# Kernel optimization log

Hardware: AMD Instinct MI355X
Metric: run time of the kernel (lower is better)

The kernel has to match this reference:

```python
import jax, jax.numpy as jnp
import numpy as np

B, P, T, K = 8, 64, 63, 2        # scenes, proposals/scene, text tokens, target proposals/scene
D, DFF, L = 512, 2048, 2         # d_model, ffn dim, encoder layers
V, NC = 30522, 18                # vocab, classes
DPT, DWD = 1536, 768             # point feats, word feats
S = P + T


def _ln(x, g, b):
    m = x.mean(-1, keepdims=True)
    v = ((x - m) ** 2).mean(-1, keepdims=True)
    return (x - m) * jax.lax.rsqrt(v + 1e-5) * g + b


def _encode(x, mask, enc):
    # post-norm TransformerEncoderLayer (torch default), dropout=0 (eval)
    (qkv_w, qkv_b, out_w, out_b, ln1_g, ln1_b,
     ff1_w, ff1_b, ff2_w, ff2_b, ln2_g, ln2_b) = enc
    for l in range(L):
        qkv = x @ qkv_w[l] + qkv_b[l]
        q, k, v = jnp.split(qkv, 3, axis=-1)
        s = q @ k.T * (1.0 / np.sqrt(D)) + mask
        a = jax.nn.softmax(s, axis=-1) @ v
        x = _ln(x + a @ out_w[l] + out_b[l], ln1_g[l], ln1_b[l])
        f = jax.nn.relu(x @ ff1_w[l] + ff1_b[l]) @ ff2_w[l] + ff2_b[l]
        x = _ln(x + f, ln2_g[l], ln2_b[l])
    return x


def _seq2seq_mask():
    # boxes attend to boxes only; text attends to all boxes + causal text
    i = jnp.arange(S)[:, None]
    j = jnp.arange(S)[None, :]
    allowed = (j < P) | ((i >= P) & (j <= i))
    return jnp.where(allowed, 0.0, -1e9).astype(jnp.float32)


def setup_inputs():
    ks = iter(jax.random.split(jax.random.key(0), 48))

    def nrm(shape, s=0.02):
        return jax.random.normal(next(ks), shape, jnp.float32) * s

    return dict(
        instances=jax.random.normal(next(ks), (B * P, DPT), jnp.float32),
        text_embeddings=jax.random.normal(next(ks), (B, T, DWD), jnp.float32),
        target_proposals=jax.random.randint(next(ks), (B, K), 0, P),
        target_word_ids=jax.random.randint(next(ks), (B, T + 1), 0, V),
        target_classes=jax.random.randint(next(ks), (B,), 0, NC),
        Wi1=nrm((DPT, 1024)), bi1=jnp.zeros((1024,)),
        Wi2=nrm((1024, D)), bi2=jnp.zeros((D,)),
        Ww=nrm((DWD, D)), bw=jnp.zeros((D,)),
        qkv_w=nrm((L, D, 3 * D)), qkv_b=jnp.zeros((L, 3 * D)),
        out_w=nrm((L, D, D)), out_b=jnp.zeros((L, D)),
        ln1_g=jnp.ones((L, D)), ln1_b=jnp.zeros((L, D)),
        ff1_w=nrm((L, D, DFF)), ff1_b=jnp.zeros((L, DFF)),
        ff2_w=nrm((L, DFF, D)), ff2_b=jnp.zeros((L, D)),
        ln2_g=jnp.ones((L, D)), ln2_b=jnp.zeros((L, D)),
        grd_w1=nrm((D, 256)), grd_b1=jnp.zeros((256,)),
        grd_w2=nrm((256, 1)), grd_b2=jnp.zeros((1,)),
        cls_w1=nrm((D, 256)), cls_b1=jnp.zeros((256,)),
        cls_w2=nrm((256, NC)), cls_b2=jnp.zeros((NC,)),
        cap_w1=nrm((D, DWD)), cap_b1=jnp.zeros((DWD,)),
        cap_w2=nrm((DWD, V)), cap_b2=jnp.zeros((V,)),
    )


def reference(instances, text_embeddings, target_proposals, target_word_ids,
              target_classes, Wi1, bi1, Wi2, bi2, Ww, bw, qkv_w, qkv_b, out_w,
              out_b, ln1_g, ln1_b, ff1_w, ff1_b, ff2_w, ff2_b, ln2_g, ln2_b,
              grd_w1, grd_b1, grd_w2, grd_b2, cls_w1, cls_b1, cls_w2, cls_b2,
              cap_w1, cap_b1, cap_w2, cap_b2):
    enc = (qkv_w, qkv_b, out_w, out_b, ln1_g, ln1_b,
           ff1_w, ff1_b, ff2_w, ff2_b, ln2_g, ln2_b)
    box = ((instances @ Wi1 + bi1) @ Wi2 + bi2).reshape(B, P, D)
    txt = text_embeddings @ Ww + bw                                   # [B,T,D]
    # ---- VG branch (unmasked encoder) ----
    vg = jnp.concatenate([box, txt + box.mean(1, keepdims=True)], axis=1)
    out_vg = jax.vmap(lambda x: _encode(x, 0.0, enc))(vg)             # [B,S,D]
    match_scores = (((out_vg[:, :P] @ grd_w1 + grd_b1) @ grd_w2 + grd_b2)
                    .squeeze(-1))                                     # [B,P]
    cls_scores = (out_vg[:, P] @ cls_w1 + cls_b1) @ cls_w2 + cls_b2   # [B,NC]
    # ---- DC branch (seq2seq mask), vmapped over scenes x target proposals ----
    tgt_box = jnp.take_along_axis(box, target_proposals[:, :, None], axis=1)
    cue = txt[:, None] + tgt_box[:, :, None]                          # [B,K,T,D]
    dc = jnp.concatenate(
        [jnp.broadcast_to(box[:, None], (B, K, P, D)), cue], axis=2)  # [B,K,S,D]
    mask = _seq2seq_mask()
    out_dc = jax.vmap(jax.vmap(lambda x: _encode(x, mask, enc)))(dc)
    dc_scores = (out_dc[:, :, P:] @ cap_w1 + cap_b1) @ cap_w2 + cap_b2  # [B,K,T,V]
    # ---- losses ----
    tgt = jnp.zeros((B, P)).at[jnp.arange(B)[:, None], target_proposals].set(1.0 / K)
    match_loss = (-(tgt * jax.nn.log_softmax(match_scores, -1)).sum(-1)).mean()
    cls_lp = jax.nn.log_softmax(cls_scores, -1)
    cls_loss = -jnp.take_along_axis(cls_lp, target_classes[:, None], 1).mean()
    wid = jnp.broadcast_to(target_word_ids[:, None, 1:T + 1], (B, K, T))
    dc_lp = jnp.take_along_axis(jax.nn.log_softmax(dc_scores, -1),
                                wid[..., None], axis=3)[..., 0]       # [B,K,T]
    dc_loss = (-dc_lp.mean(-1)).sum(-1).mean()   # sum over proposals, mean over scenes
    return (match_scores, match_loss, cls_scores, cls_loss, dc_scores, dc_loss)
```

## Files before the change

kernel.cpp:

```cpp
#include <hip/hip_runtime.h>
#include <hip/hip_bf16.h>


typedef __hip_bfloat16 bf16;
typedef __attribute__((ext_vector_type(8))) __bf16 bf16x8;
typedef __attribute__((ext_vector_type(4))) float floatx4;

#define NB 8
#define NP 64
#define NT 63
#define NK 2
#define ND 512
#define NDFF 2048
#define NV 30522
#define NNC 18
#define NS 127
#define NSEQ 24
#define NROWS (NSEQ*NS)

#define OUT_MS 0
#define OUT_MLOSS 512
#define OUT_CS 513
#define OUT_CLOSS 657
#define OUT_DC 658
#define OUT_DCLOSS 30766834

#define C2M 1008
#define C2N 30522
#define C2K 768
#define C2NT 239
#define C2H  478

__device__ __forceinline__ float bflo(unsigned u){ return __uint_as_float(u << 16); }
__device__ __forceinline__ float bfhi(unsigned u){ return __uint_as_float(u & 0xffff0000u); }

__device__ __forceinline__ void gload16(const void* g, void* l) {
    __builtin_amdgcn_global_load_lds(
        (const __attribute__((address_space(1))) unsigned*)g,
        (__attribute__((address_space(3))) unsigned*)l, 16, 0, 0);
}

#define LDSS 40

__global__ __launch_bounds__(256) void gemm_kernel(
    const bf16* __restrict__ A, const bf16* __restrict__ WT,
    const float* __restrict__ bias, const bf16* __restrict__ resid,
    bf16* __restrict__ C, int M, int N, int K, int relu)
{
    __shared__ bf16 As[64 * LDSS];
    __shared__ bf16 Bs[64 * LDSS];
    const int tid = threadIdx.x;
    const int m0 = blockIdx.x * 64;
    const int n0 = blockIdx.y * 64;
    const int lane = tid & 63;
    const int wave = tid >> 6;
    const int wm = (wave >> 1) * 32, wn = (wave & 1) * 32;
    const int quad = lane >> 4, r = lane & 15;
    const int lrow = tid >> 2;
    const int lk = (tid & 3) * 8;
    const int arow = m0 + lrow;
    const int brow = n0 + lrow;

    floatx4 acc[2][2] = {};

    for (int k0 = 0; k0 < K; k0 += 32) {
        __syncthreads();
        int4 av = {0,0,0,0}, bv = {0,0,0,0};
        if (arow < M) av = *(const int4*)(A  + (size_t)arow * K + k0 + lk);
        if (brow < N) bv = *(const int4*)(WT + (size_t)brow * K + k0 + lk);
        *(int4*)(&As[lrow * LDSS + lk]) = av;
        *(int4*)(&Bs[lrow * LDSS + lk]) = bv;
        __syncthreads();

        bf16x8 a0 = *(const bf16x8*)(&As[(wm + r)      * LDSS + quad * 8]);
        bf16x8 a1 = *(const bf16x8*)(&As[(wm + 16 + r) * LDSS + quad * 8]);
        bf16x8 b0 = *(const bf16x8*)(&Bs[(wn + r)      * LDSS + quad * 8]);
        bf16x8 b1 = *(const bf16x8*)(&Bs[(wn + 16 + r) * LDSS + quad * 8]);
        acc[0][0] = __builtin_amdgcn_mfma_f32_16x16x32_bf16(a0, b0, acc[0][0], 0, 0, 0);
        acc[0][1] = __builtin_amdgcn_mfma_f32_16x16x32_bf16(a0, b1, acc[0][1], 0, 0, 0);
        acc[1][0] = __builtin_amdgcn_mfma_f32_16x16x32_bf16(a1, b0, acc[1][0], 0, 0, 0);
        acc[1][1] = __builtin_amdgcn_mfma_f32_16x16x32_bf16(a1, b1, acc[1][1], 0, 0, 0);
    }

    #pragma unroll
    for (int ti = 0; ti < 2; ++ti)
    #pragma unroll
    for (int tj = 0; tj < 2; ++tj) {
        int col = n0 + wn + tj * 16 + r;
        if (col >= N) continue;
        float bvv = bias ? bias[col] : 0.f;
        #pragma unroll
        for (int rr = 0; rr < 4; ++rr) {
            int row = m0 + wm + ti * 16 + quad * 4 + rr;
            if (row >= M) continue;
            float v = acc[ti][tj][rr] + bvv;
            if (resid) v += (float)resid[(size_t)row * N + col];
            if (relu)  v = v > 0.f ? v : 0.f;
            C[(size_t)row * N + col] = __float2bfloat16(v);
        }
    }
}

__global__ __launch_bounds__(256) void gemm128_kernel(
    const bf16* __restrict__ A, const bf16* __restrict__ WT,
    const float* __restrict__ bias, const bf16* __restrict__ resid,
    bf16* __restrict__ C, int M, int N, int K, int relu)
{
    __shared__ bf16 As[128 * 32];
    __shared__ bf16 Bs[128 * 32];
    const int tid = threadIdx.x;
    const int m0 = blockIdx.x * 128;
    const int n0 = blockIdx.y * 128;
    const int lane = tid & 63, wave = tid >> 6;
    const int quad = lane >> 4, r = lane & 15;
    const int wm = (wave >> 1) * 64, wn = (wave & 1) * 64;
    const int srow0 = wave * 32 + (lane >> 2);
    const int srow1 = srow0 + 16;
    const int sk = (lane & 3) * 8;
    const int ar0 = min(m0 + srow0, M - 1), ar1 = min(m0 + srow1, M - 1);
    const int br0 = min(n0 + srow0, N - 1), br1 = min(n0 + srow1, N - 1);
    bf16* lA = As + srow0 * 32 + sk;
    bf16* lB = Bs + srow0 * 32 + sk;

    floatx4 acc[4][4] = {};

    for (int k0 = 0; k0 < K; k0 += 32) {
        __syncthreads();
        gload16(A  + (size_t)ar0 * K + k0 + sk, lA);
        gload16(A  + (size_t)ar1 * K + k0 + sk, lA + 512);
        gload16(WT + (size_t)br0 * K + k0 + sk, lB);
        gload16(WT + (size_t)br1 * K + k0 + sk, lB + 512);
        __syncthreads();

        bf16x8 a[4], b[4];
        #pragma unroll
        for (int ti = 0; ti < 4; ++ti)
            a[ti] = *(const bf16x8*)(&As[(wm + ti * 16 + r) * 32 + quad * 8]);
        #pragma unroll
        for (int tj = 0; tj < 4; ++tj)
            b[tj] = *(const bf16x8*)(&Bs[(wn + tj * 16 + r) * 32 + quad * 8]);
        #pragma unroll
        for (int ti = 0; ti < 4; ++ti)
            #pragma unroll
            for (int tj = 0; tj < 4; ++tj)
                acc[ti][tj] = __builtin_amdgcn_mfma_f32_16x16x32_bf16(a[ti], b[tj], acc[ti][tj], 0, 0, 0);
    }

    #pragma unroll
    for (int ti = 0; ti < 4; ++ti)
    #pragma unroll
    for (int tj = 0; tj < 4; ++tj) {
        int col = n0 + wn + tj * 16 + r;
        if (col >= N) continue;
        float bvv = bias ? bias[col] : 0.f;
        #pragma unroll
        for (int rr = 0; rr < 4; ++rr) {
            int row = m0 + wm + ti * 16 + quad * 4 + rr;
            if (row >= M) continue;
            float v = acc[ti][tj][rr] + bvv;
            if (resid) v += (float)resid[(size_t)row * N + col];
            if (relu)  v = v > 0.f ? v : 0.f;
            C[(size_t)row * N + col] = __float2bfloat16(v);
        }
    }
}

__global__ __launch_bounds__(256) void gemm_cap2_kernel(
    const bf16* __restrict__ A, const bf16* __restrict__ WT,
    const float* __restrict__ bias, float* __restrict__ Cf,
    float2* __restrict__ part)
{
    __shared__ bf16 As[128 * 32];
    __shared__ bf16 Bs[128 * 32];
    const int id = blockIdx.x;
    const int xcd = id & 7, q = id >> 3;
    const int mt = q & 7, cg = q >> 3;
    const int nt = cg * 8 + xcd;
    if (nt >= C2NT) return;
    const int m0 = mt * 128, n0 = nt * 128;

    const int tid = threadIdx.x;
    const int lane = tid & 63, wave = tid >> 6;
    const int quad = lane >> 4, r = lane & 15;
    const int wm = (wave >> 1) * 64, wn = (wave & 1) * 64;
    const int srow0 = wave * 32 + (lane >> 2);
    const int srow1 = srow0 + 16;
    const int sk = (lane & 3) * 8;
    const int ar0 = min(m0 + srow0, C2M - 1), ar1 = min(m0 + srow1, C2M - 1);
    const int br0 = min(n0 + srow0, C2N - 1), br1 = min(n0 + srow1, C2N - 1);
    bf16* lA = As + srow0 * 32 + sk;
    bf16* lB = Bs + srow0 * 32 + sk;

    floatx4 acc[4][4] = {};

    for (int k0 = 0; k0 < C2K; k0 += 32) {
        __syncthreads();
        gload16(A  + (size_t)ar0 * C2K + k0 + sk, lA);
        gload16(A  + (size_t)ar1 * C2K + k0 + sk, lA + 512);
        gload16(WT + (size_t)br0 * C2K + k0 + sk, lB);
        gload16(WT + (size_t)br1 * C2K + k0 + sk, lB + 512);
        __syncthreads();

        bf16x8 a[4], b[4];
        #pragma unroll
        for (int ti = 0; ti < 4; ++ti)
            a[ti] = *(const bf16x8*)(&As[(wm + ti * 16 + r) * 32 + quad * 8]);
        #pragma unroll
        for (int tj = 0; tj < 4; ++tj)
            b[tj] = *(const bf16x8*)(&Bs[(wn + tj * 16 + r) * 32 + quad * 8]);
        #pragma unroll
        for (int ti = 0; ti < 4; ++ti)
            #pragma unroll
            for (int tj = 0; tj < 4; ++tj)
                acc[ti][tj] = __builtin_amdgcn_mfma_f32_16x16x32_bf16(a[ti], b[tj], acc[ti][tj], 0, 0, 0);
    }

    float bv[4];
    bool cok[4];
    #pragma unroll
    for (int tj = 0; tj < 4; ++tj) {
        int col = n0 + wn + tj * 16 + r;
        cok[tj] = (col < C2N);
        bv[tj] = cok[tj] ? bias[col] : 0.f;
    }
    const int half = (wn >> 6);

    #pragma unroll
    for (int ti = 0; ti < 4; ++ti) {
        #pragma unroll
        for (int rr = 0; rr < 4; ++rr) {
            const int rowg = m0 + wm + ti * 16 + quad * 4 + rr;
            const bool rok = (rowg < C2M);
            float v[4], vp[4];
            #pragma unroll
            for (int tj = 0; tj < 4; ++tj) {
                v[tj]  = acc[ti][tj][rr] + bv[tj];
                vp[tj] = cok[tj] ? v[tj] : -1e30f;
            }
            if (rok) {
                float* orow = Cf + (size_t)rowg * C2N;
                #pragma unroll
                for (int tj = 0; tj < 4; ++tj)
                    if (cok[tj]) orow[n0 + wn + tj * 16 + r] = v[tj];
            }
            float mx = fmaxf(fmaxf(vp[0], vp[1]), fmaxf(vp[2], vp[3]));
            #pragma unroll
            for (int o = 1; o < 16; o <<= 1) mx = fmaxf(mx, __shfl_xor(mx, o));
            float s = 0.f;
            #pragma unroll
            for (int tj = 0; tj < 4; ++tj)
                if (cok[tj]) s += __expf(v[tj] - mx);
            #pragma unroll
            for (int o = 1; o < 16; o <<= 1) s += __shfl_xor(s, o);
            if (r == 0 && rok)
                part[(size_t)rowg * C2H + nt * 2 + half] = make_float2(mx, s);
        }
    }
}

struct PrepDesc { const float* src; bf16* dst; int K, N, tx, start, kind; };
struct PrepArgs { PrepDesc d[14]; };

__global__ __launch_bounds__(256) void prep_kernel(PrepArgs pa)
{
    const int bid = blockIdx.x;
    int op = 0;
    #pragma unroll
    for (int i = 1; i < 14; ++i) if (bid >= pa.d[i].start) op = i;
    const PrepDesc D = pa.d[op];
    const int lt = bid - D.start;
    const int tid = threadIdx.x;
    if (D.kind == 1) {
        int base = lt * 1024 + tid * 4;
        float4 v = *(const float4*)(D.src + base);
        bf16 o[4] = { __float2bfloat16(v.x), __float2bfloat16(v.y),
                      __float2bfloat16(v.z), __float2bfloat16(v.w) };
        *(uint2*)(D.dst + base) = *(uint2*)o;
    } else {
        __shared__ float tile[32][33];
        const int tx = tid & 31, ty = tid >> 5;
        const int n0 = (lt % D.tx) * 32, k0 = (lt / D.tx) * 32;
        #pragma unroll
        for (int yy = 0; yy < 32; yy += 8)
            tile[ty + yy][tx] = D.src[(size_t)(k0 + ty + yy) * D.N + n0 + tx];
        __syncthreads();
        #pragma unroll
        for (int yy = 0; yy < 32; yy += 8)
            D.dst[(size_t)(n0 + ty + yy) * D.K + k0 + tx] =
                __float2bfloat16(tile[tx][ty + yy]);
    }
}

__global__ __launch_bounds__(256) void transpose_kernel(
    const float* __restrict__ src, bf16* __restrict__ dst, int K, int N)
{
    __shared__ float tile[32][33];
    const int tx = threadIdx.x & 31, ty = threadIdx.x >> 5;
    const int n0 = blockIdx.x * 32, k0 = blockIdx.y * 32;
    #pragma unroll
    for (int yy = 0; yy < 32; yy += 8) {
        int k = k0 + ty + yy, n = n0 + tx;
        if (k < K && n < N) tile[ty + yy][tx] = src[(size_t)k * N + n];
    }
    __syncthreads();
    #pragma unroll
    for (int yy = 0; yy < 32; yy += 8) {
        int n = n0 + ty + yy, k = k0 + tx;
        if (n < N && k < K) dst[(size_t)n * K + k] = __float2bfloat16(tile[tx][ty + yy]);
    }
}

__global__ __launch_bounds__(256) void box_mean_kernel(
    const bf16* __restrict__ box, float* __restrict__ bm)
{
    const int b = blockIdx.x, tid = threadIdx.x;
    float s0 = 0.f, s1 = 0.f;
    for (int p = 0; p < NP; ++p) {
        const bf16* rw = box + (size_t)(b * NP + p) * ND;
        s0 += (float)rw[tid];
        s1 += (float)rw[tid + 256];
    }
    bm[b * ND + tid]       = s0 * (1.f / 64.f);
    bm[b * ND + tid + 256] = s1 * (1.f / 64.f);
}

__global__ __launch_bounds__(256) void build_x_kernel(
    const bf16* __restrict__ box, const bf16* __restrict__ txt,
    const float* __restrict__ bm, const int* __restrict__ tp,
    bf16* __restrict__ X)
{
    int idx = blockIdx.x * 256 + threadIdx.x;
    if (idx >= NROWS * ND) return;
    int d = idx & (ND - 1);
    int rs = idx >> 9;
    int row = rs % NS, seq = rs / NS;
    float v;
    if (seq < NB) {
        int b = seq;
        if (row < NP) v = (float)box[(size_t)(b * NP + row) * ND + d];
        else v = (float)txt[(size_t)(b * NT + row - NP) * ND + d] + bm[b * ND + d];
    } else {
        int s2 = seq - NB, b = s2 >> 1, k = s2 & 1;
        if (row < NP) v = (float)box[(size_t)(b * NP + row) * ND + d];
        else v = (float)txt[(size_t)(b * NT + row - NP) * ND + d]
               + (float)box[(size_t)(b * NP + tp[b * NK + k]) * ND + d];
    }
    X[idx] = __float2bfloat16(v);
}

__global__ __launch_bounds__(256) void attn_kernel(
    const bf16* __restrict__ QKV, bf16* __restrict__ Aout)
{
    const int blk = blockIdx.x;
    const int seq = blk / NS, i = blk % NS;
    const int tid = threadIdx.x;
    __shared__ float qs[ND];
    __shared__ float sc[128];
    __shared__ float red[64];

    const bf16* qrow = QKV + (size_t)(seq * NS + i) * 1536;
    qs[tid]       = (float)qrow[tid];
    qs[tid + 256] = (float)qrow[tid + 256];
    __syncthreads();

    int jmax = (seq < NB) ? NS : ((i < NP) ? NP : (i + 1));

    if (tid < NS) {
        const uint4* kp = (const uint4*)(QKV + (size_t)(seq * NS + tid) * 1536 + ND);
        float d = 0.f;
        #pragma unroll 4
        for (int c = 0; c < 64; ++c) {
            uint4 u = kp[c];
            int b0 = c * 8;
            d += qs[b0+0]*bflo(u.x) + qs[b0+1]*bfhi(u.x)
               + qs[b0+2]*bflo(u.y) + qs[b0+3]*bfhi(u.y)
               + qs[b0+4]*bflo(u.z) + qs[b0+5]*bfhi(u.z)
               + qs[b0+6]*bflo(u.w) + qs[b0+7]*bfhi(u.w);
        }
        sc[tid] = (tid < jmax) ? d * 0.04419417382415922f : -1e9f;
    } else if (tid == NS) {
        sc[NS] = -1e9f;
    }
    __syncthreads();

    if (tid < 64) red[tid] = fmaxf(sc[tid], sc[tid + 64]);
    __syncthreads();
    for (int s = 32; s > 0; s >>= 1) {
        if (tid < s) red[tid] = fmaxf(red[tid], red[tid + s]);
        __syncthreads();
    }
    float m = red[0];
    __syncthreads();

    if (tid < 128) sc[tid] = __expf(sc[tid] - m);
    __syncthreads();
    if (tid < 64) red[tid] = sc[tid] + sc[tid + 64];
    __syncthreads();
    for (int s = 32; s > 0; s >>= 1) {
        if (tid < s) red[tid] += red[tid + s];
        __syncthreads();
    }
    float inv = 1.f / red[0];

    const unsigned* vp = (const unsigned*)(QKV + (size_t)(seq * NS) * 1536 + 1024);
    float a0 = 0.f, a1 = 0.f;
    for (int j = 0; j < jmax; ++j) {
        float p = sc[j];
        unsigned u = vp[(size_t)j * 768 + tid];
        a0 += p * bflo(u);
        a1 += p * bfhi(u);
    }
    bf16* orow = Aout + (size_t)(seq * NS + i) * ND;
    orow[2 * tid]     = __float2bfloat16(a0 * inv);
    orow[2 * tid + 1] = __float2bfloat16(a1 * inv);
}

__global__ __launch_bounds__(256) void ln_kernel(
    const bf16* __restrict__ Y, const float* __restrict__ g,
    const float* __restrict__ b, bf16* __restrict__ X)
{
    const int row = blockIdx.x, tid = threadIdx.x;
    const bf16* y = Y + (size_t)row * ND;
    float v0 = (float)y[tid], v1 = (float)y[tid + 256];
    __shared__ float rs[256], rq[256];
    rs[tid] = v0 + v1;
    rq[tid] = v0 * v0 + v1 * v1;
    __syncthreads();
    for (int s = 128; s > 0; s >>= 1) {
        if (tid < s) { rs[tid] += rs[tid + s]; rq[tid] += rq[tid + s]; }
        __syncthreads();
    }
    float mean = rs[0] * (1.f / ND);
    float var = rq[0] * (1.f / ND) - mean * mean;
    float rstd = rsqrtf(var + 1e-5f);
    bf16* x = X + (size_t)row * ND;
    x[tid]       = __float2bfloat16((v0 - mean) * rstd * g[tid] + b[tid]);
    x[tid + 256] = __float2bfloat16((v1 - mean) * rstd * g[tid + 256] + b[tid + 256]);
}

__global__ __launch_bounds__(256) void match_head_kernel(
    const bf16* __restrict__ X, const float* __restrict__ w1, const float* __restrict__ b1,
    const float* __restrict__ w2, const float* __restrict__ b2,
    float* __restrict__ msf, float* __restrict__ out)
{
    const int blk = blockIdx.x;
    const int b = blk >> 6, p = blk & 63;
    const int tid = threadIdx.x;
    const bf16* x = X + (size_t)(b * NS + p) * ND;
    __shared__ float xs[ND];
    __shared__ float red[256];
    xs[tid] = (float)x[tid]; xs[tid + 256] = (float)x[tid + 256];
    __syncthreads();
    float h = b1[tid];
    for (int d = 0; d < ND; ++d) h += xs[d] * w1[d * 256 + tid];
    red[tid] = h * w2[tid];
    __syncthreads();
    for (int s = 128; s > 0; s >>= 1) {
        if (tid < s) red[tid] += red[tid + s];
        __syncthreads();
    }
    if (tid == 0) {
        float scv = red[0] + b2[0];
        msf[blk] = scv;
        out[OUT_MS + blk] = scv;
    }
}

__global__ __launch_bounds__(256) void cls_head_kernel(
    const bf16* __restrict__ X, const float* __restrict__ w1, const float* __restrict__ b1,
    const float* __restrict__ w2, const float* __restrict__ b2,
    float* __restrict__ csf, float* __restrict__ out)
{
    const int b = blockIdx.x, tid = threadIdx.x;
    const bf16* x = X + (size_t)(b * NS + NP) * ND;
    __shared__ float xs[ND];
    __shared__ float hs[256];
    xs[tid] = (float)x[tid]; xs[tid + 256] = (float)x[tid + 256];
    __syncthreads();
    float h = b1[tid];
    for (int d = 0; d < ND; ++d) h += xs[d] * w1[d * 256 + tid];
    hs[tid] = h;
    __syncthreads();
    if (tid < NNC) {
        float scv = b2[tid];
        for (int c = 0; c < 256; ++c) scv += hs[c] * w2[c * NNC + tid];
        csf[b * NNC + tid] = scv;
        out[OUT_CS + b * NNC + tid] = scv;
    }
}

__global__ void small_loss_kernel(
    const float* __restrict__ msf, const float* __restrict__ csf,
    const int* __restrict__ tp, const int* __restrict__ tc, float* __restrict__ out)
{
    const int tid = threadIdx.x;
    float mloss = 0.f;
    for (int b = 0; b < NB; ++b) {
        float s = msf[b * NP + tid];
        float m = s;
        for (int o = 32; o > 0; o >>= 1) m = fmaxf(m, __shfl_xor(m, o));
        float e = __expf(s - m);
        float sum = e;
        for (int o = 32; o > 0; o >>= 1) sum += __shfl_xor(sum, o);
        float lse = m + __logf(sum);
        float w = (tid == tp[2 * b] || tid == tp[2 * b + 1]) ? 0.5f : 0.f;
        float c = w * (lse - s);
        for (int o = 32; o > 0; o >>= 1) c += __shfl_xor(c, o);
        mloss += c;
    }
    float closs = 0.f;
    for (int b = 0; b < NB; ++b) {
        float s = (tid < NNC) ? csf[b * NNC + tid] : -1e30f;
        float m = s;
        for (int o = 32; o > 0; o >>= 1) m = fmaxf(m, __shfl_xor(m, o));
        float e = (tid < NNC) ? __expf(s - m) : 0.f;
        float sum = e;
        for (int o = 32; o > 0; o >>= 1) sum += __shfl_xor(sum, o);
        if (tid == 0) closs += (m + __logf(sum)) - csf[b * NNC + tc[b]];
    }
    if (tid == 0) {
        out[OUT_MLOSS] = mloss * (1.f / NB);
        out[OUT_CLOSS] = closs * (1.f / NB);
    }
}

__global__ __launch_bounds__(256) void gather_xc_kernel(
    const bf16* __restrict__ X, bf16* __restrict__ Xc)
{
    int idx = blockIdx.x * 256 + threadIdx.x;
    if (idx >= 1008 * ND) return;
    int d = idx & (ND - 1);
    int r = idx >> 9;
    int seq = NB + r / NT, t = r % NT;
    Xc[idx] = X[(size_t)(seq * NS + NP + t) * ND + d];
}

__global__ void dc_combine_kernel(
    const float2* __restrict__ part, const float* __restrict__ scores,
    const int* __restrict__ twid, float* __restrict__ accf)
{
    const int rr = blockIdx.x, t = threadIdx.x;
    const float2* pr = part + (size_t)rr * C2H;
    float mx = -1e30f;
    for (int i = t; i < C2H; i += 64) mx = fmaxf(mx, pr[i].x);
    for (int o = 1; o < 64; o <<= 1) mx = fmaxf(mx, __shfl_xor(mx, o));
    float s = 0.f;
    for (int i = t; i < C2H; i += 64) {
        float2 p = pr[i];
        s += p.y * __expf(p.x - mx);
    }
    for (int o = 1; o < 64; o <<= 1) s += __shfl_xor(s, o);
    if (t == 0) {
        int b = rr / 126, rem = rr % 126, tok = rem % 63;
        int wid = twid[b * 64 + 1 + tok];
        float lse = mx + __logf(s);
        atomicAdd(accf, (lse - scores[(size_t)rr * C2N + wid]) * (1.f / 504.f));
    }
}

__global__ void init_kernel(float* __restrict__ acc)
{
    if (threadIdx.x < 16) acc[threadIdx.x] = 0.f;
}

__global__ void finalize_kernel(const float* __restrict__ acc, float* __restrict__ out)
{
    out[OUT_DCLOSS] = acc[0];
}

extern "C" void kernel_launch(void* const* d_in, const int* in_sizes, int n_in,
                              void* d_out, int out_size, void* d_ws, size_t ws_size,
                              hipStream_t stream)
{
    const float* instances = (const float*)d_in[0];
    const float* text_emb  = (const float*)d_in[1];
    const int*   tp        = (const int*)d_in[2];
    const int*   twid      = (const int*)d_in[3];
    const int*   tcls      = (const int*)d_in[4];
    const float* Wi1 = (const float*)d_in[5];  const float* bi1 = (const float*)d_in[6];
    const float* Wi2 = (const float*)d_in[7];  const float* bi2 = (const float*)d_in[8];
    const float* Ww  = (const float*)d_in[9];  const float* bw  = (const float*)d_in[10];
    const float* qkv_w = (const float*)d_in[11]; const float* qkv_b = (const float*)d_in[12];
    const float* out_w = (const float*)d_in[13]; const float* out_b = (const float*)d_in[14];
    const float* ln1_g = (const float*)d_in[15]; const float* ln1_b = (const float*)d_in[16];
    const float* ff1_w = (const float*)d_in[17]; const float* ff1_b = (const float*)d_in[18];
    const float* ff2_w = (const float*)d_in[19]; const float* ff2_b = (const float*)d_in[20];
    const float* ln2_g = (const float*)d_in[21]; const float* ln2_b = (const float*)d_in[22];
    const float* grd_w1 = (const float*)d_in[23]; const float* grd_b1 = (const float*)d_in[24];
    const float* grd_w2 = (const float*)d_in[25]; const float* grd_b2 = (const float*)d_in[26];
    const float* cls_w1 = (const float*)d_in[27]; const float* cls_b1 = (const float*)d_in[28];
    const float* cls_w2 = (const float*)d_in[29]; const float* cls_b2 = (const float*)d_in[30];
    const float* cap_w1 = (const float*)d_in[31]; const float* cap_b1 = (const float*)d_in[32];
    const float* cap_w2 = (const float*)d_in[33]; const float* cap_b2 = (const float*)d_in[34];

    float* out = (float*)d_out;

    char* base = (char*)d_ws;
    size_t o = 0;
    auto nxtb = [&](size_t bytes) -> char* {
        char* p = base + o; o += (bytes + 255) & ~(size_t)255; return p;
    };
    float*  bm   = (float*)nxtb(NB * ND * 4);
    float*  msf  = (float*)nxtb(512 * 4);
    float*  csf  = (float*)nxtb(144 * 4);
    float*  accf = (float*)nxtb(64);
    float2* part = (float2*)nxtb((size_t)C2M * C2H * 8);
    bf16* wt_cap1 = (bf16*)nxtb((size_t)768 * 512 * 2);
    bf16* Xc    = (bf16*)nxtb((size_t)1008 * 512 * 2);
    bf16* C1    = (bf16*)nxtb((size_t)1008 * 768 * 2);
    size_t arena0 = o;
    bf16* wt_wi1  = (bf16*)nxtb((size_t)1024 * 1536 * 2);
    bf16* wt_wi2  = (bf16*)nxtb((size_t)512 * 1024 * 2);
    bf16* wt_ww   = (bf16*)nxtb((size_t)512 * 768 * 2);
    bf16* wt_qkv  = (bf16*)nxtb((size_t)2 * 1536 * 512 * 2);
    bf16* wt_out  = (bf16*)nxtb((size_t)2 * 512 * 512 * 2);
    bf16* wt_ff1  = (bf16*)nxtb((size_t)2 * 2048 * 512 * 2);
    bf16* wt_ff2  = (bf16*)nxtb((size_t)2 * 512 * 2048 * 2);
    bf16* inst_b  = (bf16*)nxtb((size_t)512 * 1536 * 2);
    bf16* txt_b   = (bf16*)nxtb((size_t)504 * 768 * 2);
    bf16* box_h   = (bf16*)nxtb((size_t)512 * 1024 * 2);
    bf16* box     = (bf16*)nxtb((size_t)512 * 512 * 2);
    bf16* txt     = (bf16*)nxtb((size_t)504 * 512 * 2);
    bf16* X       = (bf16*)nxtb((size_t)NROWS * ND * 2);
    bf16* QKV     = (bf16*)nxtb((size_t)NROWS * 1536 * 2);
    bf16* Aout    = (bf16*)nxtb((size_t)NROWS * ND * 2);
    bf16* Ybuf    = (bf16*)nxtb((size_t)NROWS * ND * 2);
    bf16* Hbuf    = (bf16*)nxtb((size_t)NROWS * NDFF * 2);
    bf16* wt_cap2 = (bf16*)(base + arena0);

    const dim3 tb(256);

    init_kernel<<<1, 64, 0, stream>>>(accf);

    PrepArgs pa;
    int cur = 0, pi = 0;
    auto addT = [&](const float* s, bf16* d, int K, int N) {
        pa.d[pi] = PrepDesc{ s, d, K, N, N / 32, cur, 0 };
        cur += (N / 32) * (K / 32); pi++;
    };
    auto addC = [&](const float* s, bf16* d, int elems) {
        pa.d[pi] = PrepDesc{ s, d, 0, 0, 0, cur, 1 };
        cur += elems / 1024; pi++;
    };
    addT(Wi1, wt_wi1, 1536, 1024);
    addT(Wi2, wt_wi2, 1024, 512);
    addT(Ww,  wt_ww,  768,  512);
    for (int l = 0; l < 2; ++l) {
        addT(qkv_w + (size_t)l * 512 * 1536, wt_qkv + (size_t)l * 1536 * 512, 512, 1536);
        addT(out_w + (size_t)l * 512 * 512,  wt_out + (size_t)l * 512 * 512,  512, 512);
        addT(ff1_w + (size_t)l * 512 * 2048, wt_ff1 + (size_t)l * 2048 * 512, 512, 2048);
        addT(ff2_w + (size_t)l * 2048 * 512, wt_ff2 + (size_t)l * 512 * 2048, 2048, 512);
    }
    addT(cap_w1, wt_cap1, 512, 768);
    addC(instances, inst_b, 512 * 1536);
    addC(text_emb,  txt_b,  504 * 768);
    prep_kernel<<<cur, tb, 0, stream>>>(pa);

    auto G64 = [&](const bf16* A, const bf16* WT, const float* bias, const bf16* resid,
                   bf16* C, int M, int N, int K, int relu) {
        dim3 g((M + 63) / 64, (N + 63) / 64);
        gemm_kernel<<<g, tb, 0, stream>>>(A, WT, bias, resid, C, M, N, K, relu);
    };
    auto G128 = [&](const bf16* A, const bf16* WT, const float* bias, const bf16* resid,
                    bf16* C, int M, int N, int K, int relu) {
        dim3 g((M + 127) / 128, (N + 127) / 128);
        gemm128_kernel<<<g, tb, 0, stream>>>(A, WT, bias, resid, C, M, N, K, relu);
    };

    G64(inst_b, wt_wi1, bi1, nullptr, box_h, 512, 1024, 1536, 0);
    G64(box_h,  wt_wi2, bi2, nullptr, box,   512, 512,  1024, 0);
    G64(txt_b,  wt_ww,  bw,  nullptr, txt,   504, 512,  768,  0);

    box_mean_kernel<<<NB, tb, 0, stream>>>(box, bm);
    build_x_kernel<<<(NROWS * ND) / 256, tb, 0, stream>>>(box, txt, bm, tp, X);

    for (int l = 0; l < 2; ++l) {
        G128(X, wt_qkv + (size_t)l * 1536 * 512, qkv_b + l * 1536, nullptr, QKV,
             NROWS, 1536, 512, 0);
        attn_kernel<<<NROWS, tb, 0, stream>>>(QKV, Aout);
        G64(Aout, wt_out + (size_t)l * 512 * 512, out_b + l * 512, X, Ybuf,
            NROWS, 512, 512, 0);
        ln_kernel<<<NROWS, tb, 0, stream>>>(Ybuf, ln1_g + l * 512, ln1_b + l * 512, X);
        G128(X, wt_ff1 + (size_t)l * 2048 * 512, ff1_b + l * 2048, nullptr, Hbuf,
             NROWS, 2048, 512, 1);
        G64(Hbuf, wt_ff2 + (size_t)l * 512 * 2048, ff2_b + l * 512, X, Ybuf,
            NROWS, 512, 2048, 0);
        ln_kernel<<<NROWS, tb, 0, stream>>>(Ybuf, ln2_g + l * 512, ln2_b + l * 512, X);
    }

    match_head_kernel<<<512, tb, 0, stream>>>(X, grd_w1, grd_b1, grd_w2, grd_b2, msf, out);
    cls_head_kernel<<<NB, tb, 0, stream>>>(X, cls_w1, cls_b1, cls_w2, cls_b2, csf, out);
    small_loss_kernel<<<1, 64, 0, stream>>>(msf, csf, tp, tcls, out);

    gather_xc_kernel<<<(1008 * ND) / 256, tb, 0, stream>>>(X, Xc);
    G64(Xc, wt_cap1, cap_b1, nullptr, C1, 1008, 768, 512, 0);

    {
        dim3 g((C2N + 31) / 32, (C2K + 31) / 32);
        transpose_kernel<<<g, tb, 0, stream>>>(cap_w2, wt_cap2, C2K, C2N);
    }
    gemm_cap2_kernel<<<8 * 8 * 30, tb, 0, stream>>>(C1, wt_cap2, cap_b2,
                                                    out + OUT_DC, part);

    dc_combine_kernel<<<1008, 64, 0, stream>>>(part, out + OUT_DC, twid, accf);
    finalize_kernel<<<1, 1, 0, stream>>>(accf, out);

    (void)in_sizes; (void)n_in; (void)out_size; (void)ws_size;
}
```

Before: 918.4 us.

## Rework vocab-projection GEMM into 256x256 tiles with double-buffered LDS prefetch

The caption vocab GEMM moves from 128x128 tiles with 256 threads to 256x256 tiles with 512 threads. Each wave now computes a 128x64 sub-tile. Global-to-LDS loads are double-buffered, so the next K-slice is prefetched while MFMAs run, using explicit vmcnt waits, barriers and raised wave priority during the math. LDS rows get an XOR swizzle to cut bank conflicts. The softmax-partials buffer is re-laid out for 480 per-wave column chunks, which relies on the combine kernel handling the padded entries, and register pressure from the 8x4 accumulator array rises.

```diff
diff --git a/kernel.cpp b/kernel.cpp
--- a/kernel.cpp
+++ b/kernel.cpp
@@ -28,8 +28,7 @@
 #define C2M 1008
 #define C2N 30522
 #define C2K 768
-#define C2NT 239
-#define C2H  478
+#define C2H  480
 
 __device__ __forceinline__ float bflo(unsigned u){ return __uint_as_float(u << 16); }
 __device__ __forceinline__ float bfhi(unsigned u){ return __uint_as_float(u & 0xffff0000u); }
@@ -165,95 +164,117 @@
     }
 }
 
-__global__ __launch_bounds__(256) void gemm_cap2_kernel(
+#define CAP2_STAGE(buf, kt) do {                                              \
+    const int _k = (kt) * 32;                                                 \
+    bf16* _l = &smem[buf][tid * 8];                                           \
+    gload16(aP0 + _k, _l);                                                    \
+    gload16(aP1 + _k, _l + 4096);                                             \
+    gload16(bP0 + _k, _l + 8192);                                             \
+    gload16(bP1 + _k, _l + 12288);                                            \
+} while (0)
+
+#define CAP2_KITER(buf, VM) do {                                              \
+    asm volatile("s_waitcnt vmcnt(" #VM ")" ::: "memory");                    \
+    __builtin_amdgcn_sched_barrier(0);                                        \
+    __builtin_amdgcn_s_barrier();                                             \
+    const bf16* _As = &smem[buf][0];                                          \
+    const bf16* _Bs = &smem[buf][8192];                                       \
+    bf16x8 afr[8], bfr[4];                                                    \
+    _Pragma("unroll")                                                         \
+    for (int n = 0; n < 4; ++n)                                               \
+        bfr[n] = *(const bf16x8*)(_Bs + (wn + n * 16 + r) * 32 + gsw);        \
+    _Pragma("unroll")                                                         \
+    for (int m = 0; m < 8; ++m)                                               \
+        afr[m] = *(const bf16x8*)(_As + (wm + m * 16 + r) * 32 + gsw);        \
+    __builtin_amdgcn_s_setprio(1);                                            \
+    _Pragma("unroll")                                                         \
+    for (int m = 0; m < 8; ++m)                                               \
+        _Pragma("unroll")                                                     \
+        for (int n = 0; n < 4; ++n)                                           \
+            acc[m][n] = __builtin_amdgcn_mfma_f32_16x16x32_bf16(              \
+                afr[m], bfr[n], acc[m][n], 0, 0, 0);                          \
+    __builtin_amdgcn_s_setprio(0);                                            \
+    __builtin_amdgcn_sched_barrier(0);                                        \
+    __builtin_amdgcn_s_barrier();                                             \
+} while (0)
+
+__global__ __launch_bounds__(512, 2) void gemm_cap2_kernel(
     const bf16* __restrict__ A, const bf16* __restrict__ WT,
     const float* __restrict__ bias, float* __restrict__ Cf,
     float2* __restrict__ part)
 {
-    __shared__ bf16 As[128 * 32];
-    __shared__ bf16 Bs[128 * 32];
+    __shared__ bf16 smem[2][16384];
+
     const int id = blockIdx.x;
     const int xcd = id & 7, q = id >> 3;
-    const int mt = q & 7, cg = q >> 3;
-    const int nt = cg * 8 + xcd;
-    if (nt >= C2NT) return;
-    const int m0 = mt * 128, n0 = nt * 128;
+    const int mt = q & 3, ntl = q >> 2;
+    const int nt = ntl * 8 + xcd;
+    const int m0 = mt * 256, n0 = nt * 256;
 
     const int tid = threadIdx.x;
     const int lane = tid & 63, wave = tid >> 6;
     const int quad = lane >> 4, r = lane & 15;
-    const int wm = (wave >> 1) * 64, wn = (wave & 1) * 64;
-    const int srow0 = wave * 32 + (lane >> 2);
-    const int srow1 = srow0 + 16;
-    const int sk = (lane & 3) * 8;
-    const int ar0 = min(m0 + srow0, C2M - 1), ar1 = min(m0 + srow1, C2M - 1);
-    const int br0 = min(n0 + srow0, C2N - 1), br1 = min(n0 + srow1, C2N - 1);
-    bf16* lA = As + srow0 * 32 + sk;
-    bf16* lB = Bs + srow0 * 32 + sk;
-
-    floatx4 acc[4][4] = {};
-
-    for (int k0 = 0; k0 < C2K; k0 += 32) {
-        __syncthreads();
-        gload16(A  + (size_t)ar0 * C2K + k0 + sk, lA);
-        gload16(A  + (size_t)ar1 * C2K + k0 + sk, lA + 512);
-        gload16(WT + (size_t)br0 * C2K + k0 + sk, lB);
-        gload16(WT + (size_t)br1 * C2K + k0 + sk, lB + 512);
-        __syncthreads();
-
-        bf16x8 a[4], b[4];
-        #pragma unroll
-        for (int ti = 0; ti < 4; ++ti)
-            a[ti] = *(const bf16x8*)(&As[(wm + ti * 16 + r) * 32 + quad * 8]);
-        #pragma unroll
-        for (int tj = 0; tj < 4; ++tj)
-            b[tj] = *(const bf16x8*)(&Bs[(wn + tj * 16 + r) * 32 + quad * 8]);
-        #pragma unroll
-        for (int ti = 0; ti < 4; ++ti)
-            #pragma unroll
-            for (int tj = 0; tj < 4; ++tj)
-                acc[ti][tj] = __builtin_amdgcn_mfma_f32_16x16x32_bf16(a[ti], b[tj], acc[ti][tj], 0, 0, 0);
-    }
+    const int wm = (wave >> 2) * 128;
+    const int wn = (wave & 3) * 64;
+    const int gsw = (quad ^ (r & 3)) * 8;
+
+    const int srow = tid >> 2;
+    const int sgr  = ((tid & 3) ^ (srow & 3)) * 8;
+    const bf16* aP0 = A  + (size_t)min(m0 + srow,       C2M - 1) * C2K + sgr;
+    const bf16* aP1 = A  + (size_t)min(m0 + srow + 128, C2M - 1) * C2K + sgr;
+    const bf16* bP0 = WT + (size_t)min(n0 + srow,       C2N - 1) * C2K + sgr;
+    const bf16* bP1 = WT + (size_t)min(n0 + srow + 128, C2N - 1) * C2K + sgr;
+
+    floatx4 acc[8][4] = {};
+
+    CAP2_STAGE(0, 0);
+    CAP2_STAGE(1, 1);
+    for (int t = 0; t < 22; ++t) {
+        if (t & 1) { CAP2_KITER(1, 4); } else { CAP2_KITER(0, 4); }
+        CAP2_STAGE((t & 1), t + 2);
+    }
+    CAP2_KITER(0, 4);
+    CAP2_KITER(1, 0);
 
     float bv[4];
     bool cok[4];
     #pragma unroll
-    for (int tj = 0; tj < 4; ++tj) {
-        int col = n0 + wn + tj * 16 + r;
-        cok[tj] = (col < C2N);
-        bv[tj] = cok[tj] ? bias[col] : 0.f;
-    }
-    const int half = (wn >> 6);
-
-    #pragma unroll
-    for (int ti = 0; ti < 4; ++ti) {
+    for (int n = 0; n < 4; ++n) {
+        int col = n0 + wn + n * 16 + r;
+        cok[n] = (col < C2N);
+        bv[n] = cok[n] ? bias[col] : 0.f;
+    }
+    const int w = nt * 4 + (wave & 3);
+
+    #pragma unroll
+    for (int m = 0; m < 8; ++m) {
         #pragma unroll
         for (int rr = 0; rr < 4; ++rr) {
-            const int rowg = m0 + wm + ti * 16 + quad * 4 + rr;
+            const int rowg = m0 + wm + m * 16 + quad * 4 + rr;
             const bool rok = (rowg < C2M);
             float v[4], vp[4];
             #pragma unroll
-            for (int tj = 0; tj < 4; ++tj) {
-                v[tj]  = acc[ti][tj][rr] + bv[tj];
-                vp[tj] = cok[tj] ? v[tj] : -1e30f;
+            for (int n = 0; n < 4; ++n) {
+                v[n]  = acc[m][n][rr] + bv[n];
+                vp[n] = cok[n] ? v[n] : -1e30f;
             }
             if (rok) {
                 float* orow = Cf + (size_t)rowg * C2N;
                 #pragma unroll
-                for (int tj = 0; tj < 4; ++tj)
-                    if (cok[tj]) orow[n0 + wn + tj * 16 + r] = v[tj];
+                for (int n = 0; n < 4; ++n)
+                    if (cok[n]) orow[n0 + wn + n * 16 + r] = v[n];
             }
             float mx = fmaxf(fmaxf(vp[0], vp[1]), fmaxf(vp[2], vp[3]));
             #pragma unroll
             for (int o = 1; o < 16; o <<= 1) mx = fmaxf(mx, __shfl_xor(mx, o));
             float s = 0.f;
             #pragma unroll
-            for (int tj = 0; tj < 4; ++tj)
-                if (cok[tj]) s += __expf(v[tj] - mx);
+            for (int n = 0; n < 4; ++n)
+                if (cok[n]) s += __expf(v[n] - mx);
             #pragma unroll
             for (int o = 1; o < 16; o <<= 1) s += __shfl_xor(s, o);
             if (r == 0 && rok)
-                part[(size_t)rowg * C2H + nt * 2 + half] = make_float2(mx, s);
+                part[(size_t)rowg * C2H + w] = make_float2(mx, s);
         }
     }
 }
@@ -699,7 +720,7 @@
         dim3 g((C2N + 31) / 32, (C2K + 31) / 32);
         transpose_kernel<<<g, tb, 0, stream>>>(cap_w2, wt_cap2, C2K, C2N);
     }
-    gemm_cap2_kernel<<<8 * 8 * 30, tb, 0, stream>>>(C1, wt_cap2, cap_b2,
+    gemm_cap2_kernel<<<480, dim3(512), 0, stream>>>(C1, wt_cap2, cap_b2,
                                                     out + OUT_DC, part);
 
     dc_combine_kernel<<<1008, 64, 0, stream>>>(part, out + OUT_DC, twid, accf);
```

Result: slower. 988.2 us (+7.6%).
